# Kernel optimization log

Measured on AMD Instinct MI355X. Metric: run time of the kernel, lower is better.

## Reference

```python
import jax, jax.numpy as jnp
import numpy as np


def setup_inputs() -> dict:
    key = jax.random.key(0)
    k1, k2 = jax.random.split(key)
    # x: [B, C_meg, T, c_in] -- NHWC where H is the MEG sensor axis (split axis 1 in original)
    x = jax.random.normal(k1, (8, 160, 1024, 1), dtype=jnp.float32)
    # W: [kh=1, kw=7, c_in=1, filters=32] conv kernel (self.conv.weights[0]; bias is never applied)
    W = jax.random.normal(k2, (1, 7, 1, 32), dtype=jnp.float32) * 0.1
    return {"x": x, "W": W}


def reference(x, W):
    # Original: for each sensor pair (i, j != i), conv2d(x_i + x_j, W), then max over j,
    # stacked over i -> [B, C, T, F].
    # Conv is linear and bias-free, so conv(x_i + x_j) = y_i + y_j where y = conv(x).
    # Hence out_i = y_i + max_{j != i} y_j  (exact algebraic rewrite, O(C) convs not O(C^2)).
    y = jax.lax.conv_general_dilated(
        x, W, window_strides=(1, 1), padding="SAME",
        dimension_numbers=("NHWC", "HWIO", "NHWC"),
    )  # [B, C, T, F] (kh=1 => per-sensor-row temporal conv, same as original per-slice conv)

    yt = jnp.moveaxis(y, 1, -1)               # [B, T, F, C]
    vals, idx = jax.lax.top_k(yt, 2)          # top-2 over sensor axis
    m1 = vals[..., 0:1]                       # global max over channels
    m2 = vals[..., 1:2]                       # second max
    am = idx[..., 0:1]                        # argmax channel
    C = yt.shape[-1]
    # max over j != i: equals m1 unless i is the argmax, then m2
    max_other = jnp.where(am == jnp.arange(C), m2, m1)  # [B, T, F, C]
    out = yt + max_other
    return jnp.moveaxis(out, -1, 1)           # [B, C, T, F]
```

## Files before the change

kernel.cpp:

```cpp
#include <hip/hip_runtime.h>


#define WT 8
#define BLOCK 256

__global__ __launch_bounds__(BLOCK)
void pcc_kernel(const float* __restrict__ x,
                const float* __restrict__ Wf,
                float* __restrict__ out) {
    __shared__ float xs[160][WT + 6];

    const int n  = blockIdx.x >> 7;
    const int wt = blockIdx.x & 127;
    const int w0 = wt * WT;
    const int tid = threadIdx.x;

    const float* xn = x + (size_t)n * 160 * 1024;
    for (int idx = tid; idx < 160 * (WT + 6); idx += BLOCK) {
        int row = idx / (WT + 6);
        int col = idx - row * (WT + 6);
        int gw  = w0 - 3 + col;
        float v = 0.f;
        if (gw >= 0 && gw < 1024) v = xn[row * 1024 + gw];
        xs[row][col] = v;
    }
    __syncthreads();

    const int c  = tid & 31;
    const int wl = tid >> 5;

    float wg[7];
#pragma unroll
    for (int k = 0; k < 7; ++k) wg[k] = Wf[k * 32 + c];

    float m1 = -INFINITY, m2 = -INFINITY;
    int am = 0;

#pragma unroll 4
    for (int h = 0; h < 160; ++h) {
        float y = 0.f;
#pragma unroll
        for (int j = 0; j < 7; ++j) y = fmaf(xs[h][wl + j], wg[j], y);
        bool g = y > m1;
        m2 = g ? m1 : fmaxf(m2, y);
        m1 = g ? y  : m1;
        am = g ? h  : am;
    }

    float* obase = out + ((size_t)(n * 160) * 1024 + (w0 + wl)) * 32 + c;
#pragma unroll 4
    for (int h = 0; h < 160; ++h) {
        float y = 0.f;
#pragma unroll
        for (int j = 0; j < 7; ++j) y = fmaf(xs[h][wl + j], wg[j], y);
        obase[(size_t)h * 1024 * 32] = y + (h == am ? m2 : m1);
    }
}

extern "C" void kernel_launch(void* const* d_in, const int* in_sizes, int n_in,
                              void* d_out, int out_size, void* d_ws, size_t ws_size,
                              hipStream_t stream) {
    const float* x  = (const float*)d_in[0];
    const float* Wf = (const float*)d_in[1];
    float* out = (float*)d_out;
    dim3 grid(8 * (1024 / WT));
    dim3 block(BLOCK);
    pcc_kernel<<<grid, block, 0, stream>>>(x, Wf, out);
}
```

Baseline: 185.2 us.

## Compute four time steps per thread with vectorized LDS window reuse

Each thread now computes four adjacent time outputs per channel, reading a 12-wide input window via three float4 LDS loads and reusing it across the four convolutions. Tiles widen to 32 time steps, so the grid shrinks to 256 blocks and the halo overhead per tile drops. This cuts LDS load instructions and redundant halo loads. The trade-off is fewer blocks and more registers, which lowers occupancy available to hide store latency.

```diff
diff --git a/kernel.cpp b/kernel.cpp
--- a/kernel.cpp
+++ b/kernel.cpp
@@ -1,59 +1,85 @@
 #include <hip/hip_runtime.h>
 
 
-#define WT 8
 #define BLOCK 256
+#define WTILE 32
+#define LDSW  40
 
 __global__ __launch_bounds__(BLOCK)
 void pcc_kernel(const float* __restrict__ x,
                 const float* __restrict__ Wf,
                 float* __restrict__ out) {
-    __shared__ float xs[160][WT + 6];
+    __shared__ __align__(16) float xs[160][LDSW];
 
-    const int n  = blockIdx.x >> 7;
-    const int wt = blockIdx.x & 127;
-    const int w0 = wt * WT;
+    const int n  = blockIdx.x >> 5;
+    const int wt = blockIdx.x & 31;
+    const int w0 = wt * WTILE;
     const int tid = threadIdx.x;
 
     const float* xn = x + (size_t)n * 160 * 1024;
-    for (int idx = tid; idx < 160 * (WT + 6); idx += BLOCK) {
-        int row = idx / (WT + 6);
-        int col = idx - row * (WT + 6);
-        int gw  = w0 - 3 + col;
+    for (int idx = tid; idx < 160 * LDSW; idx += BLOCK) {
+        int row = idx / LDSW;
+        int col = idx - row * LDSW;
+        int gw  = w0 - 4 + col;
         float v = 0.f;
         if (gw >= 0 && gw < 1024) v = xn[row * 1024 + gw];
         xs[row][col] = v;
     }
     __syncthreads();
 
-    const int c  = tid & 31;
-    const int wl = tid >> 5;
+    const int c = tid & 31;
+    const int t = tid >> 5;
 
     float wg[7];
 #pragma unroll
     for (int k = 0; k < 7; ++k) wg[k] = Wf[k * 32 + c];
 
-    float m1 = -INFINITY, m2 = -INFINITY;
-    int am = 0;
 
-#pragma unroll 4
+    float m1[4], m2[4];
+    int   am[4];
+#pragma unroll
+    for (int k = 0; k < 4; ++k) { m1[k] = -INFINITY; m2[k] = -INFINITY; am[k] = 0; }
+
+#pragma unroll 2
     for (int h = 0; h < 160; ++h) {
-        float y = 0.f;
+        const float* row = &xs[h][4 * t];
+        float4 A = *reinterpret_cast<const float4*>(row);
+        float4 B = *reinterpret_cast<const float4*>(row + 4);
+        float4 C = *reinterpret_cast<const float4*>(row + 8);
+        float f[12] = {A.x, A.y, A.z, A.w, B.x, B.y, B.z, B.w, C.x, C.y, C.z, C.w};
+        float y[4];
 #pragma unroll
-        for (int j = 0; j < 7; ++j) y = fmaf(xs[h][wl + j], wg[j], y);
-        bool g = y > m1;
-        m2 = g ? m1 : fmaxf(m2, y);
-        m1 = g ? y  : m1;
-        am = g ? h  : am;
+        for (int k = 0; k < 4; ++k) {
+            float acc = 0.f;
+#pragma unroll
+            for (int j = 0; j < 7; ++j) acc = fmaf(f[k + 1 + j], wg[j], acc);
+            y[k] = acc;
+        }
+#pragma unroll
+        for (int k = 0; k < 4; ++k) {
+            bool g = y[k] > m1[k];
+            m2[k] = g ? m1[k] : fmaxf(m2[k], y[k]);
+            m1[k] = g ? y[k]  : m1[k];
+            am[k] = g ? h     : am[k];
+        }
     }
 
-    float* obase = out + ((size_t)(n * 160) * 1024 + (w0 + wl)) * 32 + c;
-#pragma unroll 4
+    float* obase = out + ((size_t)(n * 160) * 1024 + (w0 + 4 * t)) * 32 + c;
+#pragma unroll 2
     for (int h = 0; h < 160; ++h) {
-        float y = 0.f;
+        const float* row = &xs[h][4 * t];
+        float4 A = *reinterpret_cast<const float4*>(row);
+        float4 B = *reinterpret_cast<const float4*>(row + 4);
+        float4 C = *reinterpret_cast<const float4*>(row + 8);
+        float f[12] = {A.x, A.y, A.z, A.w, B.x, B.y, B.z, B.w, C.x, C.y, C.z, C.w};
+        float* orow = obase + (size_t)h * 1024 * 32;
 #pragma unroll
-        for (int j = 0; j < 7; ++j) y = fmaf(xs[h][wl + j], wg[j], y);
-        obase[(size_t)h * 1024 * 32] = y + (h == am ? m2 : m1);
+        for (int k = 0; k < 4; ++k) {
+            float acc = 0.f;
+#pragma unroll
+            for (int j = 0; j < 7; ++j) acc = fmaf(f[k + 1 + j], wg[j], acc);
+            orow[k * 32] = acc + (h == am[k] ? m2[k] : m1[k]);
+        }
     }
 }
 
@@ -63,7 +89,7 @@
     const float* x  = (const float*)d_in[0];
     const float* Wf = (const float*)d_in[1];
     float* out = (float*)d_out;
-    dim3 grid(8 * (1024 / WT));
+    dim3 grid(8 * (1024 / WTILE));
     dim3 block(BLOCK);
     pcc_kernel<<<grid, block, 0, stream>>>(x, Wf, out);
 }
```

After: 198.2 us. 1.07x slower.

## Split into top-2 reduction pass and row-major float4 emit pass via workspace

Applied to the files above, without the earlier changes.

Replaces the single kernel with two. The first kernel computes per-(n,w,c) max, second max and argmax tables into workspace, and each thread now handles two time steps. The second kernel runs one block per (n,h) row, recomputes the conv and writes contiguous float4 outputs, instead of the old strided stores that jumped 128KB per h. This costs an extra launch and table traffic of about 3MB. If the workspace is too small, the original single kernel is used as a fallback.

```diff
diff --git a/kernel.cpp b/kernel.cpp
--- a/kernel.cpp
+++ b/kernel.cpp
@@ -1,43 +1,169 @@
 #include <hip/hip_runtime.h>
 
 
-#define WT 8
-#define BLOCK 256
-
-__global__ __launch_bounds__(BLOCK)
-void pcc_kernel(const float* __restrict__ x,
+#define NW 1024
+#define NH 160
+#define NC 32
+
+#define AWT   16
+#define ALDSW 24
+
+__global__ __launch_bounds__(256)
+void pcc_pass1(const float* __restrict__ x,
+               const float* __restrict__ Wf,
+               float* __restrict__ m1t,
+               float* __restrict__ m2t,
+               int* __restrict__ amt) {
+    __shared__ __align__(16) float xs[NH][ALDSW];
+
+    const int n  = blockIdx.x >> 6;
+    const int wt = blockIdx.x & 63;
+    const int w0 = wt * AWT;
+    const int tid = threadIdx.x;
+
+    const float* xn = x + (size_t)n * NH * NW;
+    for (int idx = tid; idx < NH * ALDSW; idx += 256) {
+        int row = idx / ALDSW;
+        int col = idx - row * ALDSW;
+        int gw  = w0 - 3 + col;
+        float v = 0.f;
+        if (gw >= 0 && gw < NW) v = xn[row * NW + gw];
+        xs[row][col] = v;
+    }
+    __syncthreads();
+
+    const int c = tid & 31;
+    const int t = tid >> 5;
+
+    float wg[7];
+#pragma unroll
+    for (int k = 0; k < 7; ++k) wg[k] = Wf[k * NC + c];
+
+    float m1a = -INFINITY, m2a = -INFINITY;
+    float m1b = -INFINITY, m2b = -INFINITY;
+    int ama = 0, amb = 0;
+
+#pragma unroll 4
+    for (int h = 0; h < NH; ++h) {
+        const float2* row = reinterpret_cast<const float2*>(&xs[h][2 * t]);
+        float2 d0 = row[0], d1 = row[1], d2 = row[2], d3 = row[3];
+        float f0 = d0.x, f1 = d0.y, f2 = d1.x, f3 = d1.y;
+        float f4 = d2.x, f5 = d2.y, f6 = d3.x, f7 = d3.y;
+        float ya = 0.f, yb = 0.f;
+        ya = fmaf(f0, wg[0], ya); yb = fmaf(f1, wg[0], yb);
+        ya = fmaf(f1, wg[1], ya); yb = fmaf(f2, wg[1], yb);
+        ya = fmaf(f2, wg[2], ya); yb = fmaf(f3, wg[2], yb);
+        ya = fmaf(f3, wg[3], ya); yb = fmaf(f4, wg[3], yb);
+        ya = fmaf(f4, wg[4], ya); yb = fmaf(f5, wg[4], yb);
+        ya = fmaf(f5, wg[5], ya); yb = fmaf(f6, wg[5], yb);
+        ya = fmaf(f6, wg[6], ya); yb = fmaf(f7, wg[6], yb);
+        bool ga = ya > m1a;
+        m2a = ga ? m1a : fmaxf(m2a, ya);
+        m1a = ga ? ya  : m1a;
+        ama = ga ? h   : ama;
+        bool gb = yb > m1b;
+        m2b = gb ? m1b : fmaxf(m2b, yb);
+        m1b = gb ? yb  : m1b;
+        amb = gb ? h   : amb;
+    }
+
+    const int o = (n * NW + w0 + 2 * t) * NC + c;
+    m1t[o] = m1a;  m1t[o + NC] = m1b;
+    m2t[o] = m2a;  m2t[o + NC] = m2b;
+    amt[o] = ama;  amt[o + NC] = amb;
+}
+
+__global__ __launch_bounds__(256)
+void pcc_emit(const float* __restrict__ x,
+              const float* __restrict__ Wf,
+              const float* __restrict__ m1t,
+              const float* __restrict__ m2t,
+              const int* __restrict__ amt,
+              float* __restrict__ out) {
+    __shared__ __align__(16) float xr[1032];
+
+    const int b = blockIdx.x;
+    const int n = b / NH;
+    const int h = b - n * NH;
+    const int tid = threadIdx.x;
+
+    const float* xrow = x + ((size_t)n * NH + h) * NW;
+    for (int j = tid; j < NW + 6; j += 256) {
+        int w = j - 3;
+        xr[j] = (w >= 0 && w < NW) ? xrow[w] : 0.f;
+    }
+    __syncthreads();
+
+    const int wl = tid >> 3;
+    const int c0 = (tid & 7) * 4;
+
+    float wg[7][4];
+#pragma unroll
+    for (int k = 0; k < 7; ++k) {
+        float4 wv = *reinterpret_cast<const float4*>(&Wf[k * NC + c0]);
+        wg[k][0] = wv.x; wg[k][1] = wv.y; wg[k][2] = wv.z; wg[k][3] = wv.w;
+    }
+
+    float* orow = out + ((size_t)(n * NH + h)) * NW * NC;
+    const int tbase = n * NW * NC;
+
+#pragma unroll 2
+    for (int j = 0; j < 32; ++j) {
+        const int w = j * 32 + wl;
+        float f[7];
+#pragma unroll
+        for (int k = 0; k < 7; ++k) f[k] = xr[w + k];
+
+        const int ti = tbase + w * NC + c0;
+        float4 m1v = *reinterpret_cast<const float4*>(&m1t[ti]);
+        float4 m2v = *reinterpret_cast<const float4*>(&m2t[ti]);
+        int4   amv = *reinterpret_cast<const int4*>(&amt[ti]);
+
+        float y0 = 0.f, y1 = 0.f, y2 = 0.f, y3 = 0.f;
+#pragma unroll
+        for (int k = 0; k < 7; ++k) {
+            y0 = fmaf(f[k], wg[k][0], y0);
+            y1 = fmaf(f[k], wg[k][1], y1);
+            y2 = fmaf(f[k], wg[k][2], y2);
+            y3 = fmaf(f[k], wg[k][3], y3);
+        }
+        float4 o;
+        o.x = y0 + (h == amv.x ? m2v.x : m1v.x);
+        o.y = y1 + (h == amv.y ? m2v.y : m1v.y);
+        o.z = y2 + (h == amv.z ? m2v.z : m1v.z);
+        o.w = y3 + (h == amv.w ? m2v.w : m1v.w);
+        *reinterpret_cast<float4*>(&orow[(size_t)w * NC + c0]) = o;
+    }
+}
+
+__global__ __launch_bounds__(256)
+void pcc_single(const float* __restrict__ x,
                 const float* __restrict__ Wf,
                 float* __restrict__ out) {
-    __shared__ float xs[160][WT + 6];
-
+    __shared__ float xs[NH][14];
     const int n  = blockIdx.x >> 7;
     const int wt = blockIdx.x & 127;
-    const int w0 = wt * WT;
+    const int w0 = wt * 8;
     const int tid = threadIdx.x;
-
-    const float* xn = x + (size_t)n * 160 * 1024;
-    for (int idx = tid; idx < 160 * (WT + 6); idx += BLOCK) {
-        int row = idx / (WT + 6);
-        int col = idx - row * (WT + 6);
+    const float* xn = x + (size_t)n * NH * NW;
+    for (int idx = tid; idx < NH * 14; idx += 256) {
+        int row = idx / 14;
+        int col = idx - row * 14;
         int gw  = w0 - 3 + col;
         float v = 0.f;
-        if (gw >= 0 && gw < 1024) v = xn[row * 1024 + gw];
+        if (gw >= 0 && gw < NW) v = xn[row * NW + gw];
         xs[row][col] = v;
     }
     __syncthreads();
-
     const int c  = tid & 31;
     const int wl = tid >> 5;
-
     float wg[7];
 #pragma unroll
-    for (int k = 0; k < 7; ++k) wg[k] = Wf[k * 32 + c];
-
+    for (int k = 0; k < 7; ++k) wg[k] = Wf[k * NC + c];
     float m1 = -INFINITY, m2 = -INFINITY;
     int am = 0;
-
 #pragma unroll 4
-    for (int h = 0; h < 160; ++h) {
+    for (int h = 0; h < NH; ++h) {
         float y = 0.f;
 #pragma unroll
         for (int j = 0; j < 7; ++j) y = fmaf(xs[h][wl + j], wg[j], y);
@@ -46,14 +172,13 @@
         m1 = g ? y  : m1;
         am = g ? h  : am;
     }
-
-    float* obase = out + ((size_t)(n * 160) * 1024 + (w0 + wl)) * 32 + c;
+    float* obase = out + ((size_t)(n * NH) * NW + (w0 + wl)) * NC + c;
 #pragma unroll 4
-    for (int h = 0; h < 160; ++h) {
+    for (int h = 0; h < NH; ++h) {
         float y = 0.f;
 #pragma unroll
         for (int j = 0; j < 7; ++j) y = fmaf(xs[h][wl + j], wg[j], y);
-        obase[(size_t)h * 1024 * 32] = y + (h == am ? m2 : m1);
+        obase[(size_t)h * NW * NC] = y + (h == am ? m2 : m1);
     }
 }
 
@@ -63,7 +188,17 @@
     const float* x  = (const float*)d_in[0];
     const float* Wf = (const float*)d_in[1];
     float* out = (float*)d_out;
-    dim3 grid(8 * (1024 / WT));
-    dim3 block(BLOCK);
-    pcc_kernel<<<grid, block, 0, stream>>>(x, Wf, out);
-}
+
+    const size_t tbl = (size_t)8 * NW * NC;
+    const size_t need = tbl * 4 * 3;
+
+    if (ws_size >= need) {
+        float* m1t = (float*)d_ws;
+        float* m2t = m1t + tbl;
+        int*   amt = (int*)(m2t + tbl);
+        pcc_pass1<<<dim3(8 * (NW / AWT)), dim3(256), 0, stream>>>(x, Wf, m1t, m2t, amt);
+        pcc_emit <<<dim3(8 * NH),         dim3(256), 0, stream>>>(x, Wf, m1t, m2t, amt, out);
+    } else {
+        pcc_single<<<dim3(8 * (NW / 8)), dim3(256), 0, stream>>>(x, Wf, out);
+    }
+}
```

New measurement: 233.1 us. 1.26x slower.
